# Kernel tuning notes

Hardware: AMD Instinct MI355X
Metric: run time of the kernel (lower is better)

Reference implementation:

```python
import jax, jax.numpy as jnp
import numpy as np

H = 1024      # hidden_size
NH = 16       # num_attention_heads
KV = 4        # num_key_value_heads
HD = 64       # head_dim
E = 16        # num_experts
K = 2         # num_experts_per_tok
F = 1024      # moe_intermediate_size
EPS = 1e-6
THETA = 10000.0
B, S = 2, 1024


def rmsnorm(x, w):
    v = x.astype(jnp.float32)
    v = v * jax.lax.rsqrt(jnp.mean(v * v, axis=-1, keepdims=True) + EPS)
    return (v * w).astype(x.dtype)


def rotate_half(x):
    h = x.shape[-1] // 2
    return jnp.concatenate([-x[..., h:], x[..., :h]], axis=-1)


def setup_inputs() -> dict:
    key = jax.random.key(0)
    ks = jax.random.split(key, 12)
    s = 0.02
    return {
        "hidden_states": jax.random.normal(ks[0], (B, S, H), jnp.float32),
        "position_ids": jnp.broadcast_to(jnp.arange(S, dtype=jnp.int32), (B, S)),
        "ln1_w": jnp.ones((H,), jnp.float32),
        "ln2_w": jnp.ones((H,), jnp.float32),
        "q_w": jax.random.normal(ks[1], (NH * HD, H), jnp.float32) * s,
        "k_w": jax.random.normal(ks[2], (KV * HD, H), jnp.float32) * s,
        "v_w": jax.random.normal(ks[3], (KV * HD, H), jnp.float32) * s,
        "o_w": jax.random.normal(ks[4], (H, NH * HD), jnp.float32) * s,
        "qn_w": jnp.ones((HD,), jnp.float32),
        "kn_w": jnp.ones((HD,), jnp.float32),
        "gate_w": jax.random.normal(ks[5], (E, H), jnp.float32) * s,
        "w_gate": jax.random.normal(ks[6], (E, F, H), jnp.float32) * s,
        "w_up": jax.random.normal(ks[7], (E, F, H), jnp.float32) * s,
        "w_down": jax.random.normal(ks[8], (E, H, F), jnp.float32) * s,
    }


def reference(hidden_states, position_ids, ln1_w, ln2_w, q_w, k_w, v_w, o_w,
              qn_w, kn_w, gate_w, w_gate, w_up, w_down):
    b, s, _ = hidden_states.shape
    # ---- attention (pre-norm, bidirectional, GQA, RoPE, q/k RMSNorm) ----
    h = rmsnorm(hidden_states, ln1_w)
    q = (h @ q_w.T).reshape(b, s, NH, HD)
    k = (h @ k_w.T).reshape(b, s, KV, HD)
    v = (h @ v_w.T).reshape(b, s, KV, HD)
    q = jnp.swapaxes(rmsnorm(q, qn_w), 1, 2)   # [b,NH,s,HD]
    k = jnp.swapaxes(rmsnorm(k, kn_w), 1, 2)   # [b,KV,s,HD]
    v = jnp.swapaxes(v, 1, 2)
    inv_freq = 1.0 / (THETA ** (jnp.arange(0, HD, 2, dtype=jnp.float32) / HD))
    freqs = position_ids.astype(jnp.float32)[..., None] * inv_freq  # [b,s,HD/2]
    emb = jnp.concatenate([freqs, freqs], axis=-1)                  # [b,s,HD]
    cos = jnp.cos(emb)[:, None]                                     # [b,1,s,HD]
    sin = jnp.sin(emb)[:, None]
    q = q * cos + rotate_half(q) * sin
    k = k * cos + rotate_half(k) * sin
    rep = NH // KV
    k = jnp.repeat(k, rep, axis=1)
    v = jnp.repeat(v, rep, axis=1)
    scores = jnp.einsum('bhqd,bhkd->bhqk', q, k) * (HD ** -0.5)
    attn = jax.nn.softmax(scores.astype(jnp.float32), axis=-1).astype(q.dtype)
    o = jnp.einsum('bhqk,bhkd->bhqd', attn, v)
    o = jnp.swapaxes(o, 1, 2).reshape(b, s, NH * HD) @ o_w.T
    x1 = hidden_states + o
    # ---- sparse MoE (pre-norm, top-k routing, silu-gated experts) ----
    h2 = rmsnorm(x1, ln2_w)
    xf = h2.reshape(-1, H)                                  # [T,H]
    logits = xf @ gate_w.T                                  # [T,E]
    probs = jax.nn.softmax(logits.astype(jnp.float32), axis=-1)
    w, sel = jax.lax.top_k(probs, K)                        # [T,K]
    w = w / jnp.sum(w, axis=-1, keepdims=True)              # norm_topk_prob
    T = xf.shape[0]
    # combine weights scattered into dense [T,E] (zero for unselected experts)
    cw = jnp.zeros((T, E), jnp.float32).at[jnp.arange(T)[:, None], sel].add(w)
    g = jnp.einsum('th,efh->tef', xf, w_gate)
    u = jnp.einsum('th,efh->tef', xf, w_up)
    a = jax.nn.silu(g) * u
    y = jnp.einsum('tef,ehf,te->th', a, w_down, cw.astype(xf.dtype))
    out = x1 + y.reshape(b, s, H)
    return out, logits.reshape(b, s, E)
```

## Files before the change

### kernel.cpp

```cpp
#include <hip/hip_runtime.h>
#include <hip/hip_bf16.h>
#include <math.h>

typedef __bf16 bf16x8 __attribute__((ext_vector_type(8)));
typedef float f32x4 __attribute__((ext_vector_type(4)));

constexpr int HID = 1024;
constexpr int NHEAD = 16;
constexpr int NKV = 4;
constexpr int HDIM = 64;
constexpr int NEXP = 16;
constexpr int FFD = 1024;
constexpr int NB = 2;
constexpr int SEQ = 1024;
constexpr int TOK = NB * SEQ;
constexpr int QKV_N = NHEAD * HDIM + 2 * NKV * HDIM;
constexpr float RMS_EPS = 1e-6f;
constexpr int LDP = 32;
constexpr int PL = 64 * LDP;
constexpr int MAXBLK = 2 * TOK / 128 + NEXP;

__device__ __forceinline__ int swz(int row, int e8) {
  return row * LDP + (e8 ^ (((row >> 1) & 3) << 3));
}

__device__ __forceinline__ void gload_lds16(const void* g, void* l) {
  __builtin_amdgcn_global_load_lds(
      (const __attribute__((address_space(1))) void*)g,
      (__attribute__((address_space(3))) void*)l, 16, 0, 0);
}

__device__ __forceinline__ void split2(float x, __bf16& h1, __bf16& h2) {
  h1 = (__bf16)x;
  h2 = (__bf16)(x - (float)h1);
}

__device__ __forceinline__ void mfma_step3(const __bf16* sm, int wr, int wc,
                                           int lm, int lq, f32x4 (&acc)[2][2]) {
  int ao0 = swz(wr + lm, lq * 8), ao1 = ao0 + 16 * LDP;
  int bo0 = swz(wc + lm, lq * 8), bo1 = bo0 + 16 * LDP;
  bf16x8 a10 = *(const bf16x8*)(sm + ao0),          a11 = *(const bf16x8*)(sm + ao1);
  bf16x8 a20 = *(const bf16x8*)(sm + PL + ao0),     a21 = *(const bf16x8*)(sm + PL + ao1);
  bf16x8 b10 = *(const bf16x8*)(sm + 2 * PL + bo0), b11 = *(const bf16x8*)(sm + 2 * PL + bo1);
  bf16x8 b20 = *(const bf16x8*)(sm + 3 * PL + bo0), b21 = *(const bf16x8*)(sm + 3 * PL + bo1);
#define MF(A, B, i, j) acc[i][j] = __builtin_amdgcn_mfma_f32_16x16x32_bf16(A, B, acc[i][j], 0, 0, 0)
  MF(a10, b10, 0, 0); MF(a10, b11, 0, 1); MF(a11, b10, 1, 0); MF(a11, b11, 1, 1);
  MF(a10, b20, 0, 0); MF(a10, b21, 0, 1); MF(a11, b20, 1, 0); MF(a11, b21, 1, 1);
  MF(a20, b10, 0, 0); MF(a20, b11, 0, 1); MF(a21, b10, 1, 0); MF(a21, b11, 1, 1);
#undef MF
}

__device__ __forceinline__ void cvt8(__bf16* dst, float4 f0, float4 f1) {
  __bf16 tmp[8] __attribute__((aligned(16))) = {
      (__bf16)f0.x, (__bf16)f0.y, (__bf16)f0.z, (__bf16)f0.w,
      (__bf16)f1.x, (__bf16)f1.y, (__bf16)f1.z, (__bf16)f1.w};
  *(int4*)dst = *(const int4*)tmp;
}


__global__ __launch_bounds__(256) void split2_kernel(
    const float* __restrict__ src, __bf16* __restrict__ p1,
    __bf16* __restrict__ p2, int n) {
  int i = (blockIdx.x * 256 + threadIdx.x) * 4;
  if (i >= n) return;
  float4 v = *(const float4*)(src + i);
  __bf16 t1[4] __attribute__((aligned(8))), t2[4] __attribute__((aligned(8)));
  split2(v.x, t1[0], t2[0]);
  split2(v.y, t1[1], t2[1]);
  split2(v.z, t1[2], t2[2]);
  split2(v.w, t1[3], t2[3]);
  *(int2*)(p1 + i) = *(const int2*)t1;
  *(int2*)(p2 + i) = *(const int2*)t2;
}

__global__ __launch_bounds__(256) void rmsnorm_split2_kernel(
    const float* __restrict__ x, const float* __restrict__ w,
    __bf16* __restrict__ p1, __bf16* __restrict__ p2) {
  int row = blockIdx.x;
  const float* xr = x + (size_t)row * HID;
  float4 v = ((const float4*)xr)[threadIdx.x];
  float ss = v.x * v.x + v.y * v.y + v.z * v.z + v.w * v.w;
  for (int off = 32; off; off >>= 1) ss += __shfl_xor(ss, off);
  __shared__ float red[4];
  int lane = threadIdx.x & 63, wid = threadIdx.x >> 6;
  if (lane == 0) red[wid] = ss;
  __syncthreads();
  float tot = red[0] + red[1] + red[2] + red[3];
  float scale = rsqrtf(tot / (float)HID + RMS_EPS);
  float4 wv = ((const float4*)w)[threadIdx.x];
  float o[4] = {v.x * scale * wv.x, v.y * scale * wv.y,
                v.z * scale * wv.z, v.w * scale * wv.w};
  __bf16 t1[4] __attribute__((aligned(8))), t2[4] __attribute__((aligned(8)));
#pragma unroll
  for (int i = 0; i < 4; i++) split2(o[i], t1[i], t2[i]);
  size_t idx = (size_t)row * HID + threadIdx.x * 4;
  *(int2*)(p1 + idx) = *(const int2*)t1;
  *(int2*)(p2 + idx) = *(const int2*)t2;
}

__global__ __launch_bounds__(256) void rmsnorm_dual_kernel(
    const float* __restrict__ x, const float* __restrict__ w,
    float* __restrict__ outf, __bf16* __restrict__ outb) {
  int row = blockIdx.x;
  const float* xr = x + (size_t)row * HID;
  float4 v = ((const float4*)xr)[threadIdx.x];
  float ss = v.x * v.x + v.y * v.y + v.z * v.z + v.w * v.w;
  for (int off = 32; off; off >>= 1) ss += __shfl_xor(ss, off);
  __shared__ float red[4];
  int lane = threadIdx.x & 63, wid = threadIdx.x >> 6;
  if (lane == 0) red[wid] = ss;
  __syncthreads();
  float tot = red[0] + red[1] + red[2] + red[3];
  float scale = rsqrtf(tot / (float)HID + RMS_EPS);
  float4 wv = ((const float4*)w)[threadIdx.x];
  float o[4] = {v.x * scale * wv.x, v.y * scale * wv.y,
                v.z * scale * wv.z, v.w * scale * wv.w};
  size_t idx = (size_t)row * HID + threadIdx.x * 4;
  *(float4*)(outf + idx) = *(const float4*)o;
  __bf16 tb[4] __attribute__((aligned(8)));
#pragma unroll
  for (int i = 0; i < 4; i++) tb[i] = (__bf16)o[i];
  *(int2*)(outb + idx) = *(const int2*)tb;
}

__global__ __launch_bounds__(256) void rope_split_kernel(
    const float* __restrict__ qkv, const int* __restrict__ pos_ids,
    const float* __restrict__ qn_w, const float* __restrict__ kn_w,
    __bf16* __restrict__ qp1, __bf16* __restrict__ qp2,
    __bf16* __restrict__ kp1, __bf16* __restrict__ kp2,
    __bf16* __restrict__ vp1, __bf16* __restrict__ vp2) {
  int t = blockIdx.x;
  int b = t >> 10, s = t & 1023;
  int lane = threadIdx.x & 63, w = threadIdx.x >> 6;
  float pos = (float)pos_ids[t];
  int fi = lane & 31;
  float inv = powf(10000.0f, -((float)(2 * fi)) / 64.0f);
  float cs = cosf(pos * inv), sn = sinf(pos * inv);
  for (int i = 0; i < 6; i++) {
    int hh = w + 4 * i;
    float val = qkv[(size_t)t * QKV_N + hh * 64 + lane];
    __bf16 h1, h2;
    if (hh < 20) {
      float ss = val * val;
      for (int off = 32; off; off >>= 1) ss += __shfl_xor(ss, off);
      float scale = rsqrtf(ss / 64.0f + RMS_EPS);
      float wgt = (hh < 16) ? qn_w[lane] : kn_w[lane];
      val = val * scale * wgt;
      float partner = __shfl_xor(val, 32);
      float rot = (lane < 32) ? -partner : partner;
      val = val * cs + rot * sn;
      split2(val, h1, h2);
      if (hh < 16) {
        size_t idx = (((size_t)b * NHEAD + hh) * SEQ + s) * HDIM + lane;
        qp1[idx] = h1; qp2[idx] = h2;
      } else {
        size_t idx = (((size_t)b * NKV + (hh - 16)) * SEQ + s) * HDIM + lane;
        kp1[idx] = h1; kp2[idx] = h2;
      }
    } else {
      split2(val, h1, h2);
      size_t idx = (((size_t)b * NKV + (hh - 20)) * HDIM + lane) * SEQ + s;
      vp1[idx] = h1; vp2[idx] = h2;
    }
  }
}

__global__ __launch_bounds__(256) void softmax2_kernel(
    const float* __restrict__ sf,
    __bf16* __restrict__ p1, __bf16* __restrict__ p2) {
  size_t roff = (size_t)blockIdx.x * SEQ;
  int tid = threadIdx.x;
  float4 v4 = *(const float4*)(sf + roff + tid * 4);
  float v[4] = {v4.x, v4.y, v4.z, v4.w};
  float mx = fmaxf(fmaxf(v[0], v[1]), fmaxf(v[2], v[3]));
  for (int off = 32; off; off >>= 1) mx = fmaxf(mx, __shfl_xor(mx, off));
  __shared__ float red[4], red2[4];
  int lane = tid & 63, wid = tid >> 6;
  if (lane == 0) red[wid] = mx;
  __syncthreads();
  mx = fmaxf(fmaxf(red[0], red[1]), fmaxf(red[2], red[3]));
  float e[4], sum = 0.f;
#pragma unroll
  for (int i = 0; i < 4; i++) { e[i] = expf(v[i] - mx); sum += e[i]; }
  for (int off = 32; off; off >>= 1) sum += __shfl_xor(sum, off);
  if (lane == 0) red2[wid] = sum;
  __syncthreads();
  sum = red2[0] + red2[1] + red2[2] + red2[3];
  float invs = 1.0f / sum;
  __bf16 t1[4] __attribute__((aligned(8))), t2[4] __attribute__((aligned(8)));
#pragma unroll
  for (int i = 0; i < 4; i++) split2(e[i] * invs, t1[i], t2[i]);
  *(int2*)(p1 + roff + tid * 4) = *(const int2*)t1;
  *(int2*)(p2 + roff + tid * 4) = *(const int2*)t2;
}


__global__ __launch_bounds__(256) void gemm_qkv4(
    const __bf16* __restrict__ a1, const __bf16* __restrict__ a2,
    const __bf16* __restrict__ b1, const __bf16* __restrict__ b2,
    float* __restrict__ qkv) {
  int m0 = blockIdx.x * 64, n0 = blockIdx.y * 64;
  __shared__ __bf16 sm[2][4 * PL];
  int tid = threadIdx.x, r = tid >> 2;
  int csw = ((tid & 3) ^ ((r >> 1) & 3)) * 8;
  size_t aoff = (size_t)(m0 + r) * HID + csw, boff = (size_t)(n0 + r) * HID + csw;
  f32x4 acc[2][2] = {};
  int lane = tid & 63, wid = tid >> 6;
  int wr = (wid >> 1) * 32, wc = (wid & 1) * 32, lq = lane >> 4, lm = lane & 15;
  auto gld4 = [&](int p, int k0) {
    gload_lds16(a1 + aoff + k0, &sm[p][0 * PL + tid * 8]);
    gload_lds16(a2 + aoff + k0, &sm[p][1 * PL + tid * 8]);
    gload_lds16(b1 + boff + k0, &sm[p][2 * PL + tid * 8]);
    gload_lds16(b2 + boff + k0, &sm[p][3 * PL + tid * 8]);
  };
  gld4(0, 0);
  __syncthreads();
  int p = 0;
  for (int k0 = 0; k0 < HID; k0 += 32, p ^= 1) {
    if (k0 + 32 < HID) gld4(p ^ 1, k0 + 32);
    mfma_step3(sm[p], wr, wc, lm, lq, acc);
    __syncthreads();
  }
#pragma unroll
  for (int mt = 0; mt < 2; mt++)
#pragma unroll
    for (int nt = 0; nt < 2; nt++)
#pragma unroll
      for (int i = 0; i < 4; i++) {
        int gm = m0 + wr + mt * 16 + lq * 4 + i;
        int gc = n0 + wc + nt * 16 + lm;
        qkv[(size_t)gm * QKV_N + gc] = acc[mt][nt][i];
      }
}

__global__ __launch_bounds__(256) void gemm_scores4(
    const __bf16* __restrict__ qp1, const __bf16* __restrict__ qp2,
    const __bf16* __restrict__ kp1, const __bf16* __restrict__ kp2,
    float* __restrict__ sf, int b, int h0) {
  int hz = blockIdx.z, h = h0 + hz;
  int m0 = blockIdx.x * 64, n0 = blockIdx.y * 64;
  size_t qbase = ((size_t)(b * NHEAD + h)) * SEQ * HDIM;
  size_t kbase = ((size_t)(b * NKV + (h >> 2))) * SEQ * HDIM;
  __shared__ __bf16 sm[2][4 * PL];
  int tid = threadIdx.x, r = tid >> 2;
  int csw = ((tid & 3) ^ ((r >> 1) & 3)) * 8;
  size_t aoff = qbase + (size_t)(m0 + r) * HDIM + csw;
  size_t boff = kbase + (size_t)(n0 + r) * HDIM + csw;
  f32x4 acc[2][2] = {};
  int lane = tid & 63, wid = tid >> 6;
  int wr = (wid >> 1) * 32, wc = (wid & 1) * 32, lq = lane >> 4, lm = lane & 15;
  auto gld4 = [&](int p, int k0) {
    gload_lds16(qp1 + aoff + k0, &sm[p][0 * PL + tid * 8]);
    gload_lds16(qp2 + aoff + k0, &sm[p][1 * PL + tid * 8]);
    gload_lds16(kp1 + boff + k0, &sm[p][2 * PL + tid * 8]);
    gload_lds16(kp2 + boff + k0, &sm[p][3 * PL + tid * 8]);
  };
  gld4(0, 0);
  __syncthreads();
  int p = 0;
  for (int k0 = 0; k0 < HDIM; k0 += 32, p ^= 1) {
    if (k0 + 32 < HDIM) gld4(p ^ 1, k0 + 32);
    mfma_step3(sm[p], wr, wc, lm, lq, acc);
    __syncthreads();
  }
#pragma unroll
  for (int mt = 0; mt < 2; mt++)
#pragma unroll
    for (int nt = 0; nt < 2; nt++)
#pragma unroll
      for (int i = 0; i < 4; i++) {
        int gm = m0 + wr + mt * 16 + lq * 4 + i;
        int gc = n0 + wc + nt * 16 + lm;
        size_t idx = ((size_t)hz * SEQ + gm) * SEQ + gc;
        sf[idx] = acc[mt][nt][i] * 0.125f;
      }
}

__global__ __launch_bounds__(256) void gemm_pv4(
    const __bf16* __restrict__ s1, const __bf16* __restrict__ s2,
    const __bf16* __restrict__ vp1, const __bf16* __restrict__ vp2,
    __bf16* __restrict__ o1, __bf16* __restrict__ o2,
    int b, int h0) {
  int hz = blockIdx.z, h = h0 + hz;
  int m0 = blockIdx.x * 64;
  size_t pbase = (size_t)hz * SEQ * SEQ;
  size_t vbase = ((size_t)(b * NKV + (h >> 2))) * HDIM * SEQ;
  __shared__ __bf16 sm[2][4 * PL];
  int tid = threadIdx.x, r = tid >> 2;
  int csw = ((tid & 3) ^ ((r >> 1) & 3)) * 8;
  size_t aoff = pbase + (size_t)(m0 + r) * SEQ + csw;
  size_t boff = vbase + (size_t)r * SEQ + csw;
  f32x4 acc[2][2] = {};
  int lane = tid & 63, wid = tid >> 6;
  int wr = (wid >> 1) * 32, wc = (wid & 1) * 32, lq = lane >> 4, lm = lane & 15;
  auto gld4 = [&](int p, int k0) {
    gload_lds16(s1 + aoff + k0, &sm[p][0 * PL + tid * 8]);
    gload_lds16(s2 + aoff + k0, &sm[p][1 * PL + tid * 8]);
    gload_lds16(vp1 + boff + k0, &sm[p][2 * PL + tid * 8]);
    gload_lds16(vp2 + boff + k0, &sm[p][3 * PL + tid * 8]);
  };
  gld4(0, 0);
  __syncthreads();
  int p = 0;
  for (int k0 = 0; k0 < SEQ; k0 += 32, p ^= 1) {
    if (k0 + 32 < SEQ) gld4(p ^ 1, k0 + 32);
    mfma_step3(sm[p], wr, wc, lm, lq, acc);
    __syncthreads();
  }
#pragma unroll
  for (int mt = 0; mt < 2; mt++)
#pragma unroll
    for (int nt = 0; nt < 2; nt++)
#pragma unroll
      for (int i = 0; i < 4; i++) {
        int gm = m0 + wr + mt * 16 + lq * 4 + i;
        int gc = wc + nt * 16 + lm;
        size_t idx = ((size_t)(b * SEQ + gm)) * HID + h * 64 + gc;
        __bf16 h1_, h2_;
        split2(acc[mt][nt][i], h1_, h2_);
        o1[idx] = h1_; o2[idx] = h2_;
      }
}

__global__ __launch_bounds__(256) void gemm_oproj4(
    const __bf16* __restrict__ a1, const __bf16* __restrict__ a2,
    const __bf16* __restrict__ b1, const __bf16* __restrict__ b2,
    const float* __restrict__ hidden, float* __restrict__ x1, float* __restrict__ outp) {
  int m0 = blockIdx.x * 64, n0 = blockIdx.y * 64;
  __shared__ __bf16 sm[2][4 * PL];
  int tid = threadIdx.x, r = tid >> 2;
  int csw = ((tid & 3) ^ ((r >> 1) & 3)) * 8;
  size_t aoff = (size_t)(m0 + r) * HID + csw, boff = (size_t)(n0 + r) * HID + csw;
  f32x4 acc[2][2] = {};
  int lane = tid & 63, wid = tid >> 6;
  int wr = (wid >> 1) * 32, wc = (wid & 1) * 32, lq = lane >> 4, lm = lane & 15;
  auto gld4 = [&](int p, int k0) {
    gload_lds16(a1 + aoff + k0, &sm[p][0 * PL + tid * 8]);
    gload_lds16(a2 + aoff + k0, &sm[p][1 * PL + tid * 8]);
    gload_lds16(b1 + boff + k0, &sm[p][2 * PL + tid * 8]);
    gload_lds16(b2 + boff + k0, &sm[p][3 * PL + tid * 8]);
  };
  gld4(0, 0);
  __syncthreads();
  int p = 0;
  for (int k0 = 0; k0 < HID; k0 += 32, p ^= 1) {
    if (k0 + 32 < HID) gld4(p ^ 1, k0 + 32);
    mfma_step3(sm[p], wr, wc, lm, lq, acc);
    __syncthreads();
  }
#pragma unroll
  for (int mt = 0; mt < 2; mt++)
#pragma unroll
    for (int nt = 0; nt < 2; nt++)
#pragma unroll
      for (int i = 0; i < 4; i++) {
        int gm = m0 + wr + mt * 16 + lq * 4 + i;
        int gc = n0 + wc + nt * 16 + lm;
        size_t idx = (size_t)gm * HID + gc;
        float val = hidden[idx] + acc[mt][nt][i];
        x1[idx] = val;
        outp[idx] = val;
      }
}


__global__ void zero_cnt_kernel(int* cnt) {
  if (threadIdx.x < NEXP) cnt[threadIdx.x] = 0;
}

__global__ __launch_bounds__(64) void gating_kernel(
    const float* __restrict__ h2f, const float* __restrict__ gw,
    float* __restrict__ logits_out, int* __restrict__ cnt,
    int* __restrict__ list, float* __restrict__ wt) {
  int t = blockIdx.x;
  int lane = threadIdx.x;
  const float* xr = h2f + (size_t)t * HID;
  float part[NEXP] = {};
  for (int k = lane; k < HID; k += 64) {
    float xv = xr[k];
#pragma unroll
    for (int e = 0; e < NEXP; e++) part[e] += xv * gw[e * HID + k];
  }
#pragma unroll
  for (int e = 0; e < NEXP; e++)
    for (int off = 32; off; off >>= 1) part[e] += __shfl_xor(part[e], off);
  if (lane < NEXP) logits_out[(size_t)t * NEXP + lane] = part[lane];
  float mx = part[0];
#pragma unroll
  for (int e = 1; e < NEXP; e++) mx = fmaxf(mx, part[e]);
  float pe[NEXP];
#pragma unroll
  for (int e = 0; e < NEXP; e++) pe[e] = expf(part[e] - mx);
  int e0 = 0; float p0 = pe[0];
#pragma unroll
  for (int e = 1; e < NEXP; e++) if (pe[e] > p0) { p0 = pe[e]; e0 = e; }
  int e1 = -1; float p1 = -1.f;
#pragma unroll
  for (int e = 0; e < NEXP; e++) if (e != e0 && pe[e] > p1) { p1 = pe[e]; e1 = e; }
  float wsum = p0 + p1;
  if (lane == 0) {
    int pos0 = atomicAdd(&cnt[e0], 1);
    list[e0 * TOK + pos0] = t;
    wt[e0 * TOK + pos0] = p0 / wsum;
    int pos1 = atomicAdd(&cnt[e1], 1);
    list[e1 * TOK + pos1] = t;
    wt[e1 * TOK + pos1] = p1 / wsum;
  }
}

__global__ void scan_kernel(const int* __restrict__ cnt, int* __restrict__ base,
                            int* __restrict__ btab, int* __restrict__ nblk) {
  if (threadIdx.x == 0 && blockIdx.x == 0) {
    int acc = 0, nb = 0;
    for (int e = 0; e < NEXP; e++) {
      base[e] = acc; acc += cnt[e];
      for (int m0 = 0; m0 < cnt[e]; m0 += 128) {
        btab[2 * nb] = e; btab[2 * nb + 1] = m0; nb++;
      }
    }
    base[NEXP] = acc;
    *nblk = nb;
  }
}

__global__ __launch_bounds__(256) void gemm_gateup3(
    const __bf16* __restrict__ h2, const float* __restrict__ w_gate,
    const float* __restrict__ w_up, const int* __restrict__ cnt,
    const int* __restrict__ base, const int* __restrict__ list,
    const int* __restrict__ btab, const int* __restrict__ nblk,
    __bf16* __restrict__ aws) {
  int slot = blockIdx.y;
  if (slot >= *nblk) return;
  int e = btab[2 * slot], m0 = btab[2 * slot + 1];
  int ce = cnt[e];
  int n0 = blockIdx.x * 64;
  int be = base[e];
  __shared__ __bf16 As[2][128 * LDP], Bg[2][PL], Bu[2][PL];
  int tid = threadIdx.x, r = tid >> 2, c8 = (tid & 3) * 8;
  int csw = ((tid & 3) ^ ((r >> 1) & 3)) * 8;
  int rx0 = m0 + r;      if (rx0 >= ce) rx0 = ce - 1;
  int rx1 = m0 + 64 + r; if (rx1 >= ce) rx1 = ce - 1;
  const __bf16* arow0 = h2 + (size_t)list[e * TOK + rx0] * HID + csw;
  const __bf16* arow1 = h2 + (size_t)list[e * TOK + rx1] * HID + csw;
  const float* bgrow = w_gate + ((size_t)e * FFD + n0 + r) * HID + c8;
  const float* burow = w_up + ((size_t)e * FFD + n0 + r) * HID + c8;
  int lane = tid & 63, wid = tid >> 6;
  int wr = (wid >> 1) * 64, wc = (wid & 1) * 32, lq = lane >> 4, lm = lane & 15;
  int sidx = swz(r, c8);
  f32x4 ag[4][2] = {}, au[4][2] = {};
  float4 rg0, rg1, ru0, ru1;
  auto gldA = [&](int p, int k0) {
    gload_lds16(arow0 + k0, &As[p][tid * 8]);
    gload_lds16(arow1 + k0, &As[p][2048 + tid * 8]);
  };
  auto preloadB = [&](int k0) {
    rg0 = *(const float4*)(bgrow + k0); rg1 = *(const float4*)(bgrow + k0 + 4);
    ru0 = *(const float4*)(burow + k0); ru1 = *(const float4*)(burow + k0 + 4);
  };
  auto stageB = [&](int p) {
    cvt8(&Bg[p][sidx], rg0, rg1);
    cvt8(&Bu[p][sidx], ru0, ru1);
  };
  auto compute = [&](int p) {
    int bo0 = swz(wc + lm, lq * 8), bo1 = bo0 + 16 * LDP;
    bf16x8 g0 = *(const bf16x8*)(&Bg[p][bo0]);
    bf16x8 g1 = *(const bf16x8*)(&Bg[p][bo1]);
    bf16x8 u0 = *(const bf16x8*)(&Bu[p][bo0]);
    bf16x8 u1 = *(const bf16x8*)(&Bu[p][bo1]);
#pragma unroll
    for (int mt = 0; mt < 4; mt++) {
      bf16x8 a = *(const bf16x8*)(&As[p][swz(wr + mt * 16 + lm, lq * 8)]);
      ag[mt][0] = __builtin_amdgcn_mfma_f32_16x16x32_bf16(a, g0, ag[mt][0], 0, 0, 0);
      ag[mt][1] = __builtin_amdgcn_mfma_f32_16x16x32_bf16(a, g1, ag[mt][1], 0, 0, 0);
      au[mt][0] = __builtin_amdgcn_mfma_f32_16x16x32_bf16(a, u0, au[mt][0], 0, 0, 0);
      au[mt][1] = __builtin_amdgcn_mfma_f32_16x16x32_bf16(a, u1, au[mt][1], 0, 0, 0);
    }
  };
  preloadB(0);
  gldA(0, 0);
  stageB(0);
  preloadB(32);
  __syncthreads();
  int p = 0;
  for (int k0 = 0; k0 < HID; k0 += 32, p ^= 1) {
    if (k0 + 32 < HID) {
      gldA(p ^ 1, k0 + 32);
      stageB(p ^ 1);
      preloadB(k0 + 64 < HID ? k0 + 64 : 0);
    }
    compute(p);
    __syncthreads();
  }
#pragma unroll
  for (int mt = 0; mt < 4; mt++)
#pragma unroll
    for (int nt = 0; nt < 2; nt++)
#pragma unroll
      for (int i = 0; i < 4; i++) {
        int lrow = m0 + wr + mt * 16 + lq * 4 + i;
        if (lrow < ce) {
          int gc = n0 + wc + nt * 16 + lm;
          float g = ag[mt][nt][i], u = au[mt][nt][i];
          float a = g / (1.0f + expf(-g)) * u;
          aws[((size_t)(be + lrow)) * FFD + gc] = (__bf16)a;
        }
      }
}

__global__ __launch_bounds__(256) void gemm_down3(
    const __bf16* __restrict__ aws, const float* __restrict__ w_down,
    const int* __restrict__ cnt, const int* __restrict__ base,
    const int* __restrict__ list, const float* __restrict__ wt,
    const int* __restrict__ btab, const int* __restrict__ nblk,
    float* __restrict__ outp) {
  int slot = blockIdx.y;
  if (slot >= *nblk) return;
  int e = btab[2 * slot], m0 = btab[2 * slot + 1];
  int ce = cnt[e];
  int n0 = blockIdx.x * 64;
  int be = base[e];
  __shared__ __bf16 As[2][128 * LDP], Bs[2][PL];
  int tid = threadIdx.x, r = tid >> 2, c8 = (tid & 3) * 8;
  int csw = ((tid & 3) ^ ((r >> 1) & 3)) * 8;
  int rx0 = m0 + r;      if (rx0 >= ce) rx0 = ce - 1;
  int rx1 = m0 + 64 + r; if (rx1 >= ce) rx1 = ce - 1;
  const __bf16* arow0 = aws + (size_t)(be + rx0) * FFD + csw;
  const __bf16* arow1 = aws + (size_t)(be + rx1) * FFD + csw;
  const float* brow = w_down + ((size_t)e * HID + n0 + r) * FFD + c8;
  int lane = tid & 63, wid = tid >> 6;
  int wr = (wid >> 1) * 64, wc = (wid & 1) * 32, lq = lane >> 4, lm = lane & 15;
  int sidx = swz(r, c8);
  f32x4 acc[4][2] = {};
  float4 rb0, rb1;
  auto gldA = [&](int p, int k0) {
    gload_lds16(arow0 + k0, &As[p][tid * 8]);
    gload_lds16(arow1 + k0, &As[p][2048 + tid * 8]);
  };
  auto preloadB = [&](int k0) {
    rb0 = *(const float4*)(brow + k0); rb1 = *(const float4*)(brow + k0 + 4);
  };
  auto stageB = [&](int p) { cvt8(&Bs[p][sidx], rb0, rb1); };
  auto compute = [&](int p) {
    int bo0 = swz(wc + lm, lq * 8), bo1 = bo0 + 16 * LDP;
    bf16x8 b0 = *(const bf16x8*)(&Bs[p][bo0]);
    bf16x8 b1 = *(const bf16x8*)(&Bs[p][bo1]);
#pragma unroll
    for (int mt = 0; mt < 4; mt++) {
      bf16x8 a = *(const bf16x8*)(&As[p][swz(wr + mt * 16 + lm, lq * 8)]);
      acc[mt][0] = __builtin_amdgcn_mfma_f32_16x16x32_bf16(a, b0, acc[mt][0], 0, 0, 0);
      acc[mt][1] = __builtin_amdgcn_mfma_f32_16x16x32_bf16(a, b1, acc[mt][1], 0, 0, 0);
    }
  };
  preloadB(0);
  gldA(0, 0);
  stageB(0);
  preloadB(32);
  __syncthreads();
  int p = 0;
  for (int k0 = 0; k0 < FFD; k0 += 32, p ^= 1) {
    if (k0 + 32 < FFD) {
      gldA(p ^ 1, k0 + 32);
      stageB(p ^ 1);
      preloadB(k0 + 64 < FFD ? k0 + 64 : 0);
    }
    compute(p);
    __syncthreads();
  }
#pragma unroll
  for (int mt = 0; mt < 4; mt++)
#pragma unroll
    for (int nt = 0; nt < 2; nt++)
#pragma unroll
      for (int i = 0; i < 4; i++) {
        int lrow = m0 + wr + mt * 16 + lq * 4 + i;
        if (lrow < ce) {
          int gc = n0 + wc + nt * 16 + lm;
          int tok = list[e * TOK + lrow];
          float wgt = wt[e * TOK + lrow];
          atomicAdd(&outp[(size_t)tok * HID + gc], wgt * acc[mt][nt][i]);
        }
      }
}


extern "C" void kernel_launch(void* const* d_in, const int* in_sizes, int n_in,
                              void* d_out, int out_size, void* d_ws, size_t ws_size,
                              hipStream_t stream) {
  const float* hidden = (const float*)d_in[0];
  const int* pos_ids = (const int*)d_in[1];
  const float* ln1_w = (const float*)d_in[2];
  const float* ln2_w = (const float*)d_in[3];
  const float* q_w = (const float*)d_in[4];
  const float* k_w = (const float*)d_in[5];
  const float* v_w = (const float*)d_in[6];
  const float* o_w = (const float*)d_in[7];
  const float* qn_w = (const float*)d_in[8];
  const float* kn_w = (const float*)d_in[9];
  const float* gate_w = (const float*)d_in[10];
  const float* w_gate = (const float*)d_in[11];
  const float* w_up = (const float*)d_in[12];
  const float* w_down = (const float*)d_in[13];
  float* outp = (float*)d_out;
  float* logits_out = outp + (size_t)TOK * HID;

  char* ws = (char*)d_ws;
  size_t off = 0;
  auto alloc = [&](size_t bytes) {
    void* p = ws + off;
    off += (bytes + 255) & ~(size_t)255;
    return p;
  };
  const size_t NWQ = (size_t)QKV_N * HID, NOW = (size_t)HID * HID;
  __bf16* wqp1 = (__bf16*)alloc(NWQ * 2); __bf16* wqp2 = (__bf16*)alloc(NWQ * 2);
  __bf16* owp1 = (__bf16*)alloc(NOW * 2); __bf16* owp2 = (__bf16*)alloc(NOW * 2);
  const size_t NH1 = (size_t)TOK * HID;
  __bf16* h1p1 = (__bf16*)alloc(NH1 * 2); __bf16* h1p2 = (__bf16*)alloc(NH1 * 2);
  float* qkvf = (float*)alloc((size_t)TOK * QKV_N * 4);
  const size_t NQ = (size_t)NB * NHEAD * SEQ * HDIM, NK = (size_t)NB * NKV * SEQ * HDIM;
  __bf16* qp1 = (__bf16*)alloc(NQ * 2); __bf16* qp2 = (__bf16*)alloc(NQ * 2);
  __bf16* kp1 = (__bf16*)alloc(NK * 2); __bf16* kp2 = (__bf16*)alloc(NK * 2);
  __bf16* vp1 = (__bf16*)alloc(NK * 2); __bf16* vp2 = (__bf16*)alloc(NK * 2);
  size_t fixed_rest = NH1 * 2 * 2  + NH1 * 4 * 2  + NH1 * 2  +
                      NEXP * 4 * 2 + (size_t)NEXP * TOK * 8 +
                      (size_t)TOK * 2 * FFD * 2 + (1 << 20);
  size_t avail = (ws_size > off + fixed_rest) ? (ws_size - off - fixed_rest) : 0;
  int hch = (avail >= (size_t)16 * SEQ * SEQ * 8) ? 16 : 8;
  const size_t NP = (size_t)hch * SEQ * SEQ;
  float* spf = (float*)alloc(NP * 4);
  __bf16* sp1 = (__bf16*)alloc(NP * 2); __bf16* sp2 = (__bf16*)alloc(NP * 2);
  __bf16* op1 = (__bf16*)alloc(NH1 * 2); __bf16* op2 = (__bf16*)alloc(NH1 * 2);
  float* x1 = (float*)alloc(NH1 * 4);
  float* h2f = (float*)alloc(NH1 * 4);
  __bf16* h2b = (__bf16*)alloc(NH1 * 2);
  int* cnt = (int*)alloc(NEXP * 4);
  int* base = (int*)alloc((NEXP + 1) * 4);
  int* list = (int*)alloc((size_t)NEXP * TOK * 4);
  float* wt = (float*)alloc((size_t)NEXP * TOK * 4);
  int* btab = (int*)alloc((size_t)MAXBLK * 2 * 4);
  int* nblk = (int*)alloc(4);
  __bf16* aws = (__bf16*)alloc((size_t)TOK * 2 * FFD * 2);
  (void)in_sizes; (void)n_in; (void)out_size;

  split2_kernel<<<1024, 256, 0, stream>>>(q_w, wqp1, wqp2, 1024 * 1024);
  split2_kernel<<<256, 256, 0, stream>>>(k_w, wqp1 + 1024 * 1024, wqp2 + 1024 * 1024,
                                         256 * 1024);
  split2_kernel<<<256, 256, 0, stream>>>(v_w, wqp1 + 1280 * 1024, wqp2 + 1280 * 1024,
                                         256 * 1024);
  split2_kernel<<<1024, 256, 0, stream>>>(o_w, owp1, owp2, 1024 * 1024);

  rmsnorm_split2_kernel<<<TOK, 256, 0, stream>>>(hidden, ln1_w, h1p1, h1p2);
  gemm_qkv4<<<dim3(TOK / 64, QKV_N / 64), 256, 0, stream>>>(
      h1p1, h1p2, wqp1, wqp2, qkvf);
  rope_split_kernel<<<TOK, 256, 0, stream>>>(qkvf, pos_ids, qn_w, kn_w,
                                             qp1, qp2, kp1, kp2, vp1, vp2);
  for (int b = 0; b < NB; b++)
    for (int hc = 0; hc < NHEAD / hch; hc++) {
      int h0 = hc * hch;
      gemm_scores4<<<dim3(SEQ / 64, SEQ / 64, hch), 256, 0, stream>>>(
          qp1, qp2, kp1, kp2, spf, b, h0);
      softmax2_kernel<<<hch * SEQ, 256, 0, stream>>>(spf, sp1, sp2);
      gemm_pv4<<<dim3(SEQ / 64, 1, hch), 256, 0, stream>>>(
          sp1, sp2, vp1, vp2, op1, op2, b, h0);
    }
  gemm_oproj4<<<dim3(TOK / 64, HID / 64), 256, 0, stream>>>(
      op1, op2, owp1, owp2, hidden, x1, outp);

  rmsnorm_dual_kernel<<<TOK, 256, 0, stream>>>(x1, ln2_w, h2f, h2b);
  zero_cnt_kernel<<<1, 64, 0, stream>>>(cnt);
  gating_kernel<<<TOK, 64, 0, stream>>>(h2f, gate_w, logits_out, cnt, list, wt);
  scan_kernel<<<1, 1, 0, stream>>>(cnt, base, btab, nblk);
  gemm_gateup3<<<dim3(FFD / 64, MAXBLK), 256, 0, stream>>>(
      h2b, w_gate, w_up, cnt, base, list, btab, nblk, aws);
  gemm_down3<<<dim3(HID / 64, MAXBLK), 256, 0, stream>>>(
      aws, w_down, cnt, base, list, wt, btab, nblk, outp);
}
```

Before: 531.9 us.

## Triple-buffer GEMM pipelines and pre-convert expert weights to bf16

All GEMM kernels move from double-buffered LDS with __syncthreads to a three-stage ring. Each stage waits with an explicit s_waitcnt vmcnt barrier, so two tiles of loads stay in flight during compute. Expert weights are now converted to bf16 once per call in a separate kernel, so the MoE GEMMs can load B with direct global-to-LDS copies instead of loading fp32 into registers and converting. This adds a full read of the expert weights plus a bf16 write every call, and uses more LDS per block, which may reduce occupancy.

```diff
diff --git a/kernel.cpp b/kernel.cpp
--- a/kernel.cpp
+++ b/kernel.cpp
@@ -20,6 +20,12 @@
 constexpr int PL = 64 * LDP;
 constexpr int MAXBLK = 2 * TOK / 128 + NEXP;
 
+#define WB(N) do { \
+  asm volatile("s_waitcnt vmcnt(" #N ") lgkmcnt(0)" ::: "memory"); \
+  __builtin_amdgcn_s_barrier(); \
+  __builtin_amdgcn_sched_barrier(0); \
+} while (0)
+
 __device__ __forceinline__ int swz(int row, int e8) {
   return row * LDP + (e8 ^ (((row >> 1) & 3) << 3));
 }
@@ -50,13 +56,6 @@
 #undef MF
 }
 
-__device__ __forceinline__ void cvt8(__bf16* dst, float4 f0, float4 f1) {
-  __bf16 tmp[8] __attribute__((aligned(16))) = {
-      (__bf16)f0.x, (__bf16)f0.y, (__bf16)f0.z, (__bf16)f0.w,
-      (__bf16)f1.x, (__bf16)f1.y, (__bf16)f1.z, (__bf16)f1.w};
-  *(int4*)dst = *(const int4*)tmp;
-}
-
 
 __global__ __launch_bounds__(256) void split2_kernel(
     const float* __restrict__ src, __bf16* __restrict__ p1,
@@ -71,6 +70,18 @@
   split2(v.w, t1[3], t2[3]);
   *(int2*)(p1 + i) = *(const int2*)t1;
   *(int2*)(p2 + i) = *(const int2*)t2;
+}
+
+__global__ __launch_bounds__(256) void cvtw_kernel(
+    const float* __restrict__ src, __bf16* __restrict__ dst, int n) {
+  int i = (blockIdx.x * 256 + threadIdx.x) * 8;
+  if (i >= n) return;
+  float4 a = *(const float4*)(src + i);
+  float4 b = *(const float4*)(src + i + 4);
+  __bf16 t[8] __attribute__((aligned(16))) = {
+      (__bf16)a.x, (__bf16)a.y, (__bf16)a.z, (__bf16)a.w,
+      (__bf16)b.x, (__bf16)b.y, (__bf16)b.z, (__bf16)b.w};
+  *(int4*)(dst + i) = *(const int4*)t;
 }
 
 __global__ __launch_bounds__(256) void rmsnorm_split2_kernel(
@@ -200,7 +211,7 @@
     const __bf16* __restrict__ b1, const __bf16* __restrict__ b2,
     float* __restrict__ qkv) {
   int m0 = blockIdx.x * 64, n0 = blockIdx.y * 64;
-  __shared__ __bf16 sm[2][4 * PL];
+  __shared__ __bf16 sm[3][4 * PL];
   int tid = threadIdx.x, r = tid >> 2;
   int csw = ((tid & 3) ^ ((r >> 1) & 3)) * 8;
   size_t aoff = (size_t)(m0 + r) * HID + csw, boff = (size_t)(n0 + r) * HID + csw;
@@ -213,14 +224,17 @@
     gload_lds16(b1 + boff + k0, &sm[p][2 * PL + tid * 8]);
     gload_lds16(b2 + boff + k0, &sm[p][3 * PL + tid * 8]);
   };
-  gld4(0, 0);
-  __syncthreads();
-  int p = 0;
-  for (int k0 = 0; k0 < HID; k0 += 32, p ^= 1) {
-    if (k0 + 32 < HID) gld4(p ^ 1, k0 + 32);
-    mfma_step3(sm[p], wr, wc, lm, lq, acc);
-    __syncthreads();
-  }
+  constexpr int NS = HID / 32;
+  gld4(0, 0); gld4(1, 32);
+  WB(4);
+  for (int k = 0; k < NS - 2; k++) {
+    gld4((k + 2) % 3, (k + 2) * 32);
+    mfma_step3(sm[k % 3], wr, wc, lm, lq, acc);
+    WB(4);
+  }
+  mfma_step3(sm[(NS - 2) % 3], wr, wc, lm, lq, acc);
+  WB(0);
+  mfma_step3(sm[(NS - 1) % 3], wr, wc, lm, lq, acc);
 #pragma unroll
   for (int mt = 0; mt < 2; mt++)
 #pragma unroll
@@ -255,14 +269,11 @@
     gload_lds16(kp1 + boff + k0, &sm[p][2 * PL + tid * 8]);
     gload_lds16(kp2 + boff + k0, &sm[p][3 * PL + tid * 8]);
   };
-  gld4(0, 0);
-  __syncthreads();
-  int p = 0;
-  for (int k0 = 0; k0 < HDIM; k0 += 32, p ^= 1) {
-    if (k0 + 32 < HDIM) gld4(p ^ 1, k0 + 32);
-    mfma_step3(sm[p], wr, wc, lm, lq, acc);
-    __syncthreads();
-  }
+  gld4(0, 0); gld4(1, 32);
+  WB(4);
+  mfma_step3(sm[0], wr, wc, lm, lq, acc);
+  WB(0);
+  mfma_step3(sm[1], wr, wc, lm, lq, acc);
 #pragma unroll
   for (int mt = 0; mt < 2; mt++)
 #pragma unroll
@@ -285,7 +296,7 @@
   int m0 = blockIdx.x * 64;
   size_t pbase = (size_t)hz * SEQ * SEQ;
   size_t vbase = ((size_t)(b * NKV + (h >> 2))) * HDIM * SEQ;
-  __shared__ __bf16 sm[2][4 * PL];
+  __shared__ __bf16 sm[3][4 * PL];
   int tid = threadIdx.x, r = tid >> 2;
   int csw = ((tid & 3) ^ ((r >> 1) & 3)) * 8;
   size_t aoff = pbase + (size_t)(m0 + r) * SEQ + csw;
@@ -299,14 +310,17 @@
     gload_lds16(vp1 + boff + k0, &sm[p][2 * PL + tid * 8]);
     gload_lds16(vp2 + boff + k0, &sm[p][3 * PL + tid * 8]);
   };
-  gld4(0, 0);
-  __syncthreads();
-  int p = 0;
-  for (int k0 = 0; k0 < SEQ; k0 += 32, p ^= 1) {
-    if (k0 + 32 < SEQ) gld4(p ^ 1, k0 + 32);
-    mfma_step3(sm[p], wr, wc, lm, lq, acc);
-    __syncthreads();
-  }
+  constexpr int NS = SEQ / 32;
+  gld4(0, 0); gld4(1, 32);
+  WB(4);
+  for (int k = 0; k < NS - 2; k++) {
+    gld4((k + 2) % 3, (k + 2) * 32);
+    mfma_step3(sm[k % 3], wr, wc, lm, lq, acc);
+    WB(4);
+  }
+  mfma_step3(sm[(NS - 2) % 3], wr, wc, lm, lq, acc);
+  WB(0);
+  mfma_step3(sm[(NS - 1) % 3], wr, wc, lm, lq, acc);
 #pragma unroll
   for (int mt = 0; mt < 2; mt++)
 #pragma unroll
@@ -327,7 +341,7 @@
     const __bf16* __restrict__ b1, const __bf16* __restrict__ b2,
     const float* __restrict__ hidden, float* __restrict__ x1, float* __restrict__ outp) {
   int m0 = blockIdx.x * 64, n0 = blockIdx.y * 64;
-  __shared__ __bf16 sm[2][4 * PL];
+  __shared__ __bf16 sm[3][4 * PL];
   int tid = threadIdx.x, r = tid >> 2;
   int csw = ((tid & 3) ^ ((r >> 1) & 3)) * 8;
   size_t aoff = (size_t)(m0 + r) * HID + csw, boff = (size_t)(n0 + r) * HID + csw;
@@ -340,14 +354,17 @@
     gload_lds16(b1 + boff + k0, &sm[p][2 * PL + tid * 8]);
     gload_lds16(b2 + boff + k0, &sm[p][3 * PL + tid * 8]);
   };
-  gld4(0, 0);
-  __syncthreads();
-  int p = 0;
-  for (int k0 = 0; k0 < HID; k0 += 32, p ^= 1) {
-    if (k0 + 32 < HID) gld4(p ^ 1, k0 + 32);
-    mfma_step3(sm[p], wr, wc, lm, lq, acc);
-    __syncthreads();
-  }
+  constexpr int NS = HID / 32;
+  gld4(0, 0); gld4(1, 32);
+  WB(4);
+  for (int k = 0; k < NS - 2; k++) {
+    gld4((k + 2) % 3, (k + 2) * 32);
+    mfma_step3(sm[k % 3], wr, wc, lm, lq, acc);
+    WB(4);
+  }
+  mfma_step3(sm[(NS - 2) % 3], wr, wc, lm, lq, acc);
+  WB(0);
+  mfma_step3(sm[(NS - 1) % 3], wr, wc, lm, lq, acc);
 #pragma unroll
   for (int mt = 0; mt < 2; mt++)
 #pragma unroll
@@ -424,8 +441,8 @@
 }
 
 __global__ __launch_bounds__(256) void gemm_gateup3(
-    const __bf16* __restrict__ h2, const float* __restrict__ w_gate,
-    const float* __restrict__ w_up, const int* __restrict__ cnt,
+    const __bf16* __restrict__ h2, const __bf16* __restrict__ wgb,
+    const __bf16* __restrict__ wub, const int* __restrict__ cnt,
     const int* __restrict__ base, const int* __restrict__ list,
     const int* __restrict__ btab, const int* __restrict__ nblk,
     __bf16* __restrict__ aws) {
@@ -435,31 +452,23 @@
   int ce = cnt[e];
   int n0 = blockIdx.x * 64;
   int be = base[e];
-  __shared__ __bf16 As[2][128 * LDP], Bg[2][PL], Bu[2][PL];
-  int tid = threadIdx.x, r = tid >> 2, c8 = (tid & 3) * 8;
+  __shared__ __bf16 As[3][128 * LDP], Bg[3][PL], Bu[3][PL];
+  int tid = threadIdx.x, r = tid >> 2;
   int csw = ((tid & 3) ^ ((r >> 1) & 3)) * 8;
   int rx0 = m0 + r;      if (rx0 >= ce) rx0 = ce - 1;
   int rx1 = m0 + 64 + r; if (rx1 >= ce) rx1 = ce - 1;
   const __bf16* arow0 = h2 + (size_t)list[e * TOK + rx0] * HID + csw;
   const __bf16* arow1 = h2 + (size_t)list[e * TOK + rx1] * HID + csw;
-  const float* bgrow = w_gate + ((size_t)e * FFD + n0 + r) * HID + c8;
-  const float* burow = w_up + ((size_t)e * FFD + n0 + r) * HID + c8;
+  const __bf16* bgrow = wgb + ((size_t)e * FFD + n0 + r) * HID + csw;
+  const __bf16* burow = wub + ((size_t)e * FFD + n0 + r) * HID + csw;
   int lane = tid & 63, wid = tid >> 6;
   int wr = (wid >> 1) * 64, wc = (wid & 1) * 32, lq = lane >> 4, lm = lane & 15;
-  int sidx = swz(r, c8);
   f32x4 ag[4][2] = {}, au[4][2] = {};
-  float4 rg0, rg1, ru0, ru1;
-  auto gldA = [&](int p, int k0) {
+  auto gld4 = [&](int p, int k0) {
     gload_lds16(arow0 + k0, &As[p][tid * 8]);
     gload_lds16(arow1 + k0, &As[p][2048 + tid * 8]);
-  };
-  auto preloadB = [&](int k0) {
-    rg0 = *(const float4*)(bgrow + k0); rg1 = *(const float4*)(bgrow + k0 + 4);
-    ru0 = *(const float4*)(burow + k0); ru1 = *(const float4*)(burow + k0 + 4);
-  };
-  auto stageB = [&](int p) {
-    cvt8(&Bg[p][sidx], rg0, rg1);
-    cvt8(&Bu[p][sidx], ru0, ru1);
+    gload_lds16(bgrow + k0, &Bg[p][tid * 8]);
+    gload_lds16(burow + k0, &Bu[p][tid * 8]);
   };
   auto compute = [&](int p) {
     int bo0 = swz(wc + lm, lq * 8), bo1 = bo0 + 16 * LDP;
@@ -476,21 +485,17 @@
       au[mt][1] = __builtin_amdgcn_mfma_f32_16x16x32_bf16(a, u1, au[mt][1], 0, 0, 0);
     }
   };
-  preloadB(0);
-  gldA(0, 0);
-  stageB(0);
-  preloadB(32);
-  __syncthreads();
-  int p = 0;
-  for (int k0 = 0; k0 < HID; k0 += 32, p ^= 1) {
-    if (k0 + 32 < HID) {
-      gldA(p ^ 1, k0 + 32);
-      stageB(p ^ 1);
-      preloadB(k0 + 64 < HID ? k0 + 64 : 0);
-    }
-    compute(p);
-    __syncthreads();
-  }
+  constexpr int NS = HID / 32;
+  gld4(0, 0); gld4(1, 32);
+  WB(4);
+  for (int k = 0; k < NS - 2; k++) {
+    gld4((k + 2) % 3, (k + 2) * 32);
+    compute(k % 3);
+    WB(4);
+  }
+  compute((NS - 2) % 3);
+  WB(0);
+  compute((NS - 1) % 3);
 #pragma unroll
   for (int mt = 0; mt < 4; mt++)
 #pragma unroll
@@ -508,7 +513,7 @@
 }
 
 __global__ __launch_bounds__(256) void gemm_down3(
-    const __bf16* __restrict__ aws, const float* __restrict__ w_down,
+    const __bf16* __restrict__ aws, const __bf16* __restrict__ wdb,
     const int* __restrict__ cnt, const int* __restrict__ base,
     const int* __restrict__ list, const float* __restrict__ wt,
     const int* __restrict__ btab, const int* __restrict__ nblk,
@@ -519,27 +524,22 @@
   int ce = cnt[e];
   int n0 = blockIdx.x * 64;
   int be = base[e];
-  __shared__ __bf16 As[2][128 * LDP], Bs[2][PL];
-  int tid = threadIdx.x, r = tid >> 2, c8 = (tid & 3) * 8;
+  __shared__ __bf16 As[3][128 * LDP], Bs[3][PL];
+  int tid = threadIdx.x, r = tid >> 2;
   int csw = ((tid & 3) ^ ((r >> 1) & 3)) * 8;
   int rx0 = m0 + r;      if (rx0 >= ce) rx0 = ce - 1;
   int rx1 = m0 + 64 + r; if (rx1 >= ce) rx1 = ce - 1;
   const __bf16* arow0 = aws + (size_t)(be + rx0) * FFD + csw;
   const __bf16* arow1 = aws + (size_t)(be + rx1) * FFD + csw;
-  const float* brow = w_down + ((size_t)e * HID + n0 + r) * FFD + c8;
+  const __bf16* brow = wdb + ((size_t)e * HID + n0 + r) * FFD + csw;
   int lane = tid & 63, wid = tid >> 6;
   int wr = (wid >> 1) * 64, wc = (wid & 1) * 32, lq = lane >> 4, lm = lane & 15;
-  int sidx = swz(r, c8);
   f32x4 acc[4][2] = {};
-  float4 rb0, rb1;
-  auto gldA = [&](int p, int k0) {
+  auto gld3 = [&](int p, int k0) {
     gload_lds16(arow0 + k0, &As[p][tid * 8]);
     gload_lds16(arow1 + k0, &As[p][2048 + tid * 8]);
-  };
-  auto preloadB = [&](int k0) {
-    rb0 = *(const float4*)(brow + k0); rb1 = *(const float4*)(brow + k0 + 4);
-  };
-  auto stageB = [&](int p) { cvt8(&Bs[p][sidx], rb0, rb1); };
+    gload_lds16(brow + k0, &Bs[p][tid * 8]);
+  };
   auto compute = [&](int p) {
     int bo0 = swz(wc + lm, lq * 8), bo1 = bo0 + 16 * LDP;
     bf16x8 b0 = *(const bf16x8*)(&Bs[p][bo0]);
@@ -551,21 +551,17 @@
       acc[mt][1] = __builtin_amdgcn_mfma_f32_16x16x32_bf16(a, b1, acc[mt][1], 0, 0, 0);
     }
   };
-  preloadB(0);
-  gldA(0, 0);
-  stageB(0);
-  preloadB(32);
-  __syncthreads();
-  int p = 0;
-  for (int k0 = 0; k0 < FFD; k0 += 32, p ^= 1) {
-    if (k0 + 32 < FFD) {
-      gldA(p ^ 1, k0 + 32);
-      stageB(p ^ 1);
-      preloadB(k0 + 64 < FFD ? k0 + 64 : 0);
-    }
-    compute(p);
-    __syncthreads();
-  }
+  constexpr int NS = FFD / 32;
+  gld3(0, 0); gld3(1, 32);
+  WB(3);
+  for (int k = 0; k < NS - 2; k++) {
+    gld3((k + 2) % 3, (k + 2) * 32);
+    compute(k % 3);
+    WB(3);
+  }
+  compute((NS - 2) % 3);
+  WB(0);
+  compute((NS - 1) % 3);
 #pragma unroll
   for (int mt = 0; mt < 4; mt++)
 #pragma unroll
@@ -613,6 +609,10 @@
   const size_t NWQ = (size_t)QKV_N * HID, NOW = (size_t)HID * HID;
   __bf16* wqp1 = (__bf16*)alloc(NWQ * 2); __bf16* wqp2 = (__bf16*)alloc(NWQ * 2);
   __bf16* owp1 = (__bf16*)alloc(NOW * 2); __bf16* owp2 = (__bf16*)alloc(NOW * 2);
+  const size_t NWE = (size_t)NEXP * FFD * HID;
+  __bf16* wgb = (__bf16*)alloc(NWE * 2);
+  __bf16* wub = (__bf16*)alloc(NWE * 2);
+  __bf16* wdb = (__bf16*)alloc(NWE * 2);
   const size_t NH1 = (size_t)TOK * HID;
   __bf16* h1p1 = (__bf16*)alloc(NH1 * 2); __bf16* h1p2 = (__bf16*)alloc(NH1 * 2);
   float* qkvf = (float*)alloc((size_t)TOK * QKV_N * 4);
@@ -647,6 +647,9 @@
   split2_kernel<<<256, 256, 0, stream>>>(v_w, wqp1 + 1280 * 1024, wqp2 + 1280 * 1024,
                                          256 * 1024);
   split2_kernel<<<1024, 256, 0, stream>>>(o_w, owp1, owp2, 1024 * 1024);
+  cvtw_kernel<<<8192, 256, 0, stream>>>(w_gate, wgb, (int)NWE);
+  cvtw_kernel<<<8192, 256, 0, stream>>>(w_up, wub, (int)NWE);
+  cvtw_kernel<<<8192, 256, 0, stream>>>(w_down, wdb, (int)NWE);
 
   rmsnorm_split2_kernel<<<TOK, 256, 0, stream>>>(hidden, ln1_w, h1p1, h1p2);
   gemm_qkv4<<<dim3(TOK / 64, QKV_N / 64), 256, 0, stream>>>(
@@ -670,7 +673,7 @@
   gating_kernel<<<TOK, 64, 0, stream>>>(h2f, gate_w, logits_out, cnt, list, wt);
   scan_kernel<<<1, 1, 0, stream>>>(cnt, base, btab, nblk);
   gemm_gateup3<<<dim3(FFD / 64, MAXBLK), 256, 0, stream>>>(
-      h2b, w_gate, w_up, cnt, base, list, btab, nblk, aws);
+      h2b, wgb, wub, cnt, base, list, btab, nblk, aws);
   gemm_down3<<<dim3(HID / 64, MAXBLK), 256, 0, stream>>>(
-      aws, w_down, cnt, base, list, wt, btab, nblk, outp);
-}
+      aws, wdb, cnt, base, list, wt, btab, nblk, outp);
+}
```

After: 615.0 us. +15.6%, slower.
